# Kernel tuning notes

Hardware: AMD Instinct MI355X
Metric: run time of the kernel (lower is better)

Reference implementation:

```python
import jax, jax.numpy as jnp
import numpy as np

HIDDEN = 4096
N_HEADS = 16
HEAD_DIM = HIDDEN // N_HEADS  # 256
ROTARY_DIM = 64
MAX_POS = 2048
INIT_RANGE = 0.02


def _create_sinusoidal_positions(num_pos, dim):
    inv_freq = 1.0 / 10000 ** (np.arange(0, dim, 2) / dim)
    sinusoid_inp = np.einsum('i,j->ij', np.arange(num_pos), inv_freq).astype('float32')
    sin, cos = np.sin(sinusoid_inp), np.cos(sinusoid_inp)
    sentinel = dim // 2 + dim % 2
    out = np.zeros((num_pos, dim), dtype=np.float32)
    out[:, :sentinel] = sin
    out[:, sentinel:] = cos
    return jnp.array(out)

EMBED_POSITIONS = _create_sinusoidal_positions(MAX_POS, ROTARY_DIM)  # [MAX_POS, ROTARY_DIM]


def _rotate_every_two(t):
    # t: [B,S,H,R] -> interleaved (-x1, x0, -x3, x2, ...)
    rot = jnp.stack((-t[..., 1::2], t[..., ::2]), axis=-1)
    return rot.reshape(rot.shape[:-2] + (-1,))


def _apply_rotary(t, sin, cos):
    # sin/cos: [B,S,R/2] -> element-wise repeat x2 along last axis -> [B,S,1,R]
    sin_p = jnp.repeat(sin[:, :, None, :], 2, axis=-1)
    cos_p = jnp.repeat(cos[:, :, None, :], 2, axis=-1)
    return t * cos_p + _rotate_every_two(t) * sin_p


def setup_inputs() -> dict:
    key = jax.random.key(0)
    k0, k1, k2, k3, k4 = jax.random.split(key, 5)
    B, S = 2, 2048
    hidden_states = jax.random.normal(k0, (B, S, HIDDEN), dtype=jnp.float32)
    attention_mask = jnp.ones((B, S), dtype=jnp.float32)
    position_ids = jnp.broadcast_to(jnp.arange(S, dtype=jnp.int32), (B, S))
    Wq = jax.random.normal(k1, (HIDDEN, HIDDEN), dtype=jnp.float32) * INIT_RANGE
    Wk = jax.random.normal(k2, (HIDDEN, HIDDEN), dtype=jnp.float32) * INIT_RANGE
    Wv = jax.random.normal(k3, (HIDDEN, HIDDEN), dtype=jnp.float32) * INIT_RANGE
    Wo = jax.random.normal(k4, (HIDDEN, HIDDEN), dtype=jnp.float32) * INIT_RANGE
    return {"hidden_states": hidden_states, "attention_mask": attention_mask,
            "position_ids": position_ids, "Wq": Wq, "Wk": Wk, "Wv": Wv, "Wo": Wo}


def reference(hidden_states, attention_mask, position_ids, Wq, Wk, Wv, Wo):
    B, S, _ = hidden_states.shape
    # QKV projections (no bias), split heads -> [B,S,H,D]
    q = (hidden_states @ Wq).reshape(B, S, N_HEADS, HEAD_DIM)
    k = (hidden_states @ Wk).reshape(B, S, N_HEADS, HEAD_DIM)
    v = (hidden_states @ Wv).reshape(B, S, N_HEADS, HEAD_DIM)

    sincos = jnp.take(EMBED_POSITIONS, position_ids, axis=0)  # [B,S,ROTARY_DIM]
    sin, cos = jnp.split(sincos, 2, axis=-1)

    # Interleaved RoPE on first ROTARY_DIM channels only
    q_rot = _apply_rotary(q[..., :ROTARY_DIM], sin, cos)
    k_rot = _apply_rotary(k[..., :ROTARY_DIM], sin, cos)
    q = jnp.concatenate([q_rot, q[..., ROTARY_DIM:]], axis=-1)
    k = jnp.concatenate([k_rot, k[..., ROTARY_DIM:]], axis=-1)

    # Combined causal + padding mask -> additive bias
    causal = jnp.tril(jnp.ones((S, S), dtype=bool))[None, None]          # [1,1,S,S]
    pad = (attention_mask > 0)[:, None, None, :]                          # [B,1,1,S]
    mask = causal & pad                                                    # [B,1,S,S]
    bias = jnp.where(mask, 0.0, jnp.finfo(jnp.float32).min).astype(jnp.float32)

    # Scaled dot-product attention (query pre-scaled, as in flax dpa_weights)
    q = q / jnp.sqrt(jnp.float32(HEAD_DIM))
    scores = jnp.einsum('bqhd,bkhd->bhqk', q, k) + bias
    attn = jax.nn.softmax(scores, axis=-1)
    out = jnp.einsum('bhqk,bkhd->bqhd', attn, v).reshape(B, S, HIDDEN)
    return out @ Wo
```

## Files before the change

### kernel.cpp

```cpp
#include <hip/hip_runtime.h>


typedef unsigned short u16;
typedef __attribute__((ext_vector_type(4))) float f32x4;
typedef __attribute__((ext_vector_type(8))) short s16x8;
typedef __attribute__((ext_vector_type(4))) unsigned short u16x4;

#define HID 4096
#define SEQ 2048
#define NMAT (4096ull * 4096ull)

__device__ __forceinline__ u16 f2bf(float x) {
  unsigned int u = __builtin_bit_cast(unsigned int, x);
  u += 0x7FFFu + ((u >> 16) & 1u);
  return (u16)(u >> 16);
}
__device__ __forceinline__ float bf2f(u16 x) {
  unsigned int u = ((unsigned int)x) << 16;
  return __builtin_bit_cast(float, u);
}
__device__ __forceinline__ void cp16(const void* g, void* l) {
  __builtin_amdgcn_global_load_lds((__attribute__((address_space(1))) void*)(g),
                                   (__attribute__((address_space(3))) void*)(l),
                                   16, 0, 0);
}

__global__ __launch_bounds__(256) void k_cvt(const float* __restrict__ src,
                                             u16* __restrict__ dst) {
  size_t i = ((size_t)blockIdx.x * 256 + threadIdx.x) * 8;
  f32x4 a = *(const f32x4*)(src + i);
  f32x4 b = *(const f32x4*)(src + i + 4);
  u16x4 o0, o1;
  o0[0] = f2bf(a[0]); o0[1] = f2bf(a[1]); o0[2] = f2bf(a[2]); o0[3] = f2bf(a[3]);
  o1[0] = f2bf(b[0]); o1[1] = f2bf(b[1]); o1[2] = f2bf(b[2]); o1[3] = f2bf(b[3]);
  *(u16x4*)(dst + i) = o0;
  *(u16x4*)(dst + i + 4) = o1;
}

__global__ __launch_bounds__(256) void k_wtrans(const float* __restrict__ W0,
                                                const float* __restrict__ W1,
                                                const float* __restrict__ W2,
                                                const float* __restrict__ W3,
                                                u16* __restrict__ WT) {
  int z = blockIdx.z;
  const float* W = (z == 0) ? W0 : (z == 1) ? W1 : (z == 2) ? W2 : W3;
  u16* T = WT + (size_t)z * NMAT;
  __shared__ u16 tile[64][70];
  int t = threadIdx.x, tx = t & 15, ty = t >> 4;
  int n0 = blockIdx.x * 64, k0 = blockIdx.y * 64;
  for (int i = 0; i < 4; i++) {
    int kl = ty + 16 * i;
    f32x4 v = *(const f32x4*)(W + (size_t)(k0 + kl) * HID + n0 + tx * 4);
    tile[kl][tx * 4 + 0] = f2bf(v[0]);
    tile[kl][tx * 4 + 1] = f2bf(v[1]);
    tile[kl][tx * 4 + 2] = f2bf(v[2]);
    tile[kl][tx * 4 + 3] = f2bf(v[3]);
  }
  __syncthreads();
  for (int i = 0; i < 4; i++) {
    int nl = ty + 16 * i;
    u16x4 o;
    o[0] = tile[tx * 4 + 0][nl];
    o[1] = tile[tx * 4 + 1][nl];
    o[2] = tile[tx * 4 + 2][nl];
    o[3] = tile[tx * 4 + 3][nl];
    *(u16x4*)(T + (size_t)(n0 + nl) * HID + k0 + tx * 4) = o;
  }
}

__global__ __launch_bounds__(256) void k_vtrans(const u16* __restrict__ V,
                                                u16* __restrict__ Vt) {
  int bh = blockIdx.z, b = bh >> 4, h = bh & 15;
  int tok0 = blockIdx.x * 64, d0 = blockIdx.y * 64;
  __shared__ u16 tile[64][70];
  int t = threadIdx.x, tx = t & 15, ty = t >> 4;
  for (int i = 0; i < 4; i++) {
    int tl = ty + 16 * i;
    u16x4 v = *(const u16x4*)(V + (size_t)(b * SEQ + tok0 + tl) * HID + h * 256 + d0 + tx * 4);
    tile[tl][tx * 4 + 0] = v[0];
    tile[tl][tx * 4 + 1] = v[1];
    tile[tl][tx * 4 + 2] = v[2];
    tile[tl][tx * 4 + 3] = v[3];
  }
  __syncthreads();
  for (int i = 0; i < 4; i++) {
    int dl = ty + 16 * i;
    u16x4 o;
    o[0] = tile[tx * 4 + 0][dl];
    o[1] = tile[tx * 4 + 1][dl];
    o[2] = tile[tx * 4 + 2][dl];
    o[3] = tile[tx * 4 + 3][dl];
    *(u16x4*)(Vt + ((size_t)bh * 256 + d0 + dl) * SEQ + tok0 + tx * 4) = o;
  }
}

template <bool QKV>
__global__ __launch_bounds__(512, 2) void k_gemm8(const u16* __restrict__ A,
                                                  const u16* __restrict__ Bt0,
                                                  u16* __restrict__ Cb0,
                                                  float* __restrict__ Cf) {
  __shared__ u16 lds[65536];
  char* lds8 = (char*)lds;
  const int t = threadIdx.x, lane = t & 63, w = t >> 6;
  const int wm = w >> 2, wn = w & 3;
  const int l15 = lane & 15, g = lane >> 4;
  int lin = blockIdx.y * 16 + blockIdx.x;
  int swz = (lin & 7) * 32 + (lin >> 3);
  const int bm = (swz >> 4) * 256, bn = (swz & 15) * 256;
  const u16* Bt = Bt0;
  u16* Cb = Cb0;
  float scale = 1.f;
  if (QKV) {
    int z = blockIdx.z;
    Bt += (size_t)z * NMAT;
    Cb += (size_t)z * NMAT;
    if (z == 0) scale = 0.0625f;
  }
  const int Px = (t * 16) ^ (((t >> 5) & 1) << 5);
  const int r_s = Px >> 6, c_s = (Px & 63) >> 1;
  const u16* gA0 = A + (size_t)(bm + r_s) * HID + c_s;
  const u16* gA1 = gA0 + 128ull * HID;
  const u16* gB0 = Bt + (size_t)(bn + r_s) * HID + c_s;
  const u16* gB1 = gB0 + 128ull * HID;
  char* stA = lds8 + w * 1024;
  char* stB = lds8 + 32768 + w * 1024;
  const int sb = ((l15 >> 3) & 1) << 5;
  const int aL0 = wm * 16384 + ((l15 * 64 + g * 16) ^ sb);
  const int bL0 = 32768 + (wn >> 1) * 16384 + ((((wn & 1) * 64 + l15) * 64 + g * 16) ^ sb);
  const int aL1 = aL0 + 65536, bL1 = bL0 + 65536;

  f32x4 acc[8][4] = {};
  s16x8 af[4][2], b0[2][2], b1[2][2];

#define STG(P, D, KT) { const u16* s_ = (P) + (size_t)(KT) * 64; \
                        cp16(s_, (D)); cp16(s_ + 32, (D) + 8192); }
#define LDA8(MH, AL) \
  _Pragma("unroll") for (int mi = 0; mi < 4; mi++) { \
    af[mi][0] = *(const s16x8*)(lds8 + (AL) + (MH) * 4096 + mi * 1024); \
    af[mi][1] = *(const s16x8*)(lds8 + (AL) + (MH) * 4096 + mi * 1024 + 8192); }
#define LDB8(BQ, NH, BL) \
  _Pragma("unroll") for (int n2 = 0; n2 < 2; n2++) { \
    BQ[n2][0] = *(const s16x8*)(lds8 + (BL) + ((NH) * 2 + n2) * 1024); \
    BQ[n2][1] = *(const s16x8*)(lds8 + (BL) + ((NH) * 2 + n2) * 1024 + 8192); }
#define MM8(MH, BQ, NH) \
  _Pragma("unroll") for (int mi = 0; mi < 4; mi++) \
  _Pragma("unroll") for (int n2 = 0; n2 < 2; n2++) { \
    acc[(MH)*4+mi][(NH)*2+n2] = __builtin_amdgcn_mfma_f32_16x16x32_bf16( \
        af[mi][0], BQ[n2][0], acc[(MH)*4+mi][(NH)*2+n2], 0, 0, 0); \
    acc[(MH)*4+mi][(NH)*2+n2] = __builtin_amdgcn_mfma_f32_16x16x32_bf16( \
        af[mi][1], BQ[n2][1], acc[(MH)*4+mi][(NH)*2+n2], 0, 0, 0); }
#define BAR() __builtin_amdgcn_s_barrier()
#define LGKM0() asm volatile("s_waitcnt lgkmcnt(0)" ::: "memory")
#define PRIO1() __builtin_amdgcn_s_setprio(1)
#define PRIO0() __builtin_amdgcn_s_setprio(0)

  STG(gB0, stB, 0); STG(gB1, stB + 16384, 0);
  STG(gA0, stA, 0); STG(gA1, stA + 16384, 0);
  STG(gB0, stB + 65536, 1); STG(gB1, stB + 65536 + 16384, 1);
  asm volatile("s_waitcnt vmcnt(4)" ::: "memory");
  BAR();

  for (int it = 0; it < 32; ++it) {
    const int k1 = 2 * it + 1;
    const int k2 = (2 * it + 2 < 64) ? 2 * it + 2 : 63;
    const int k3 = (2 * it + 3 < 64) ? 2 * it + 3 : 63;
    LDA8(0, aL0); LDB8(b0, 0, bL0); STG(gA0, stA + 65536, k1);
    BAR(); LGKM0(); PRIO1(); MM8(0, b0, 0); PRIO0(); BAR();
    LDB8(b1, 1, bL0); STG(gA1, stA + 65536 + 16384, k1);
    BAR(); LGKM0(); PRIO1(); MM8(0, b1, 1); PRIO0(); BAR();
    LDA8(1, aL0); STG(gB0, stB, k2);
    BAR(); LGKM0(); PRIO1(); MM8(1, b1, 1); PRIO0(); BAR();
    STG(gB1, stB + 16384, k2);
    BAR(); PRIO1(); MM8(1, b0, 0); PRIO0();
    asm volatile("s_waitcnt vmcnt(4)" ::: "memory");
    BAR();
    LDA8(0, aL1); LDB8(b0, 0, bL1); STG(gA0, stA, k2);
    BAR(); LGKM0(); PRIO1(); MM8(0, b0, 0); PRIO0(); BAR();
    LDB8(b1, 1, bL1); STG(gA1, stA + 16384, k2);
    BAR(); LGKM0(); PRIO1(); MM8(0, b1, 1); PRIO0(); BAR();
    LDA8(1, aL1); STG(gB0, stB + 65536, k3);
    BAR(); LGKM0(); PRIO1(); MM8(1, b1, 1); PRIO0(); BAR();
    STG(gB1, stB + 65536 + 16384, k3);
    BAR(); PRIO1(); MM8(1, b0, 0); PRIO0();
    asm volatile("s_waitcnt vmcnt(4)" ::: "memory");
    BAR();
  }
  asm volatile("s_waitcnt vmcnt(0)" ::: "memory");
#pragma unroll
  for (int mi = 0; mi < 8; mi++)
#pragma unroll
    for (int ni = 0; ni < 4; ni++) {
      const int ml = bm + wm * 128 + mi * 16 + g * 4;
      const int nl = bn + wn * 64 + ni * 16 + l15;
#pragma unroll
      for (int rr = 0; rr < 4; rr++) {
        float v = acc[mi][ni][rr];
        if (QKV)
          Cb[(size_t)(ml + rr) * HID + nl] = f2bf(v * scale);
        else
          Cf[(size_t)(ml + rr) * HID + nl] = v;
      }
    }
#undef STG
#undef LDA8
#undef LDB8
#undef MM8
#undef BAR
#undef LGKM0
#undef PRIO1
#undef PRIO0
}

__global__ __launch_bounds__(256) void k_rope(u16* __restrict__ Q, u16* __restrict__ K,
                                              const int* __restrict__ pid) {
  int i = blockIdx.x * 256 + threadIdx.x;
  int m = i >> 9, rem = i & 511, h = rem >> 5, p = rem & 31;
  int pos = pid[m];
  double inv = pow(10000.0, -(double)p / 32.0);
  double ang = (double)pos * inv;
  float sv = (float)sin(ang), cv = (float)cos(ang);
  size_t idx = (size_t)m * HID + h * 256 + 2 * p;
  {
    unsigned int qp = *(const unsigned int*)(Q + idx);
    float a = bf2f((u16)qp), b = bf2f((u16)(qp >> 16));
    unsigned int o = (unsigned int)f2bf(a * cv - b * sv) |
                     ((unsigned int)f2bf(b * cv + a * sv) << 16);
    *(unsigned int*)(Q + idx) = o;
  }
  {
    unsigned int kp = *(const unsigned int*)(K + idx);
    float a = bf2f((u16)kp), b = bf2f((u16)(kp >> 16));
    unsigned int o = (unsigned int)f2bf(a * cv - b * sv) |
                     ((unsigned int)f2bf(b * cv + a * sv) << 16);
    *(unsigned int*)(K + idx) = o;
  }
}

__global__ __launch_bounds__(256, 2) void k_flash(const u16* __restrict__ Q,
                                                  const u16* __restrict__ Kg,
                                                  const u16* __restrict__ Vt,
                                                  const float* __restrict__ am,
                                                  u16* __restrict__ O) {
  __shared__ u16 smem[36864];
  u16* sK = smem;
  u16* sV = smem + 16384;
  u16* sP = smem + 32768;
  const int t = threadIdx.x, lane = t & 63, w = t >> 6;
  const int qt = gridDim.x - 1 - blockIdx.x;
  const int q0 = qt * 64;
  const int bh = blockIdx.y, b = bh >> 4, h = bh & 15;
  const size_t tokb = (size_t)b * SEQ;
  const int ch0 = h * 256;

  for (int j = 0; j < 8; j++) {
    int fc = j * 256 + t;
    int r = fc >> 5, cs = fc & 31, cg = cs ^ (r & 7);
    cp16(Q + (tokb + q0 + r) * (size_t)HID + ch0 + cg * 8, sK + j * 2048 + w * 512);
  }
  __syncthreads();
  s16x8 qf[8];
  {
    int rq = w * 16 + (lane & 15);
    for (int kf = 0; kf < 8; kf++) {
      int cs = ((lane >> 4) + 4 * kf) ^ (rq & 7);
      qf[kf] = *(const s16x8*)(sK + rq * 256 + cs * 8);
    }
  }
  f32x4 oacc[16] = {};
  float mrow[4], lrow[4];
  for (int rr = 0; rr < 4; rr++) { mrow[rr] = -1e30f; lrow[rr] = 0.f; }

  const int ntiles = qt + 1;
  for (int it = 0; it < ntiles; it++) {
    const int kt0 = it * 64;
    __syncthreads();
    for (int j = 0; j < 8; j++) {
      int fc = j * 256 + t;
      int r = fc >> 5, cs = fc & 31, cg = cs ^ (r & 7);
      cp16(Kg + (tokb + kt0 + r) * (size_t)HID + ch0 + cg * 8, sK + j * 2048 + w * 512);
    }
    for (int j = 0; j < 8; j++) {
      int fc = j * 256 + t;
      int rd = fc >> 3, cs = fc & 7, cg = cs ^ (rd & 7);
      cp16(Vt + ((size_t)bh * 256 + rd) * SEQ + kt0 + cg * 8, sV + j * 2048 + w * 512);
    }
    __syncthreads();
    f32x4 sacc[4] = {};
    for (int kf = 0; kf < 8; kf++) {
      s16x8 bf[4];
      for (int ni = 0; ni < 4; ni++) {
        int rk = ni * 16 + (lane & 15);
        int cs = ((lane >> 4) + 4 * kf) ^ (rk & 7);
        bf[ni] = *(const s16x8*)(sK + rk * 256 + cs * 8);
      }
      for (int ni = 0; ni < 4; ni++)
        sacc[ni] = __builtin_amdgcn_mfma_f32_16x16x32_bf16(qf[kf], bf[ni], sacc[ni], 0, 0, 0);
    }
    float amv[4];
    for (int ni = 0; ni < 4; ni++) amv[ni] = am[b * SEQ + kt0 + ni * 16 + (lane & 15)];
    const bool tail = (kt0 + 64 > q0);
    {
      int rbase = q0 + w * 16 + ((lane >> 4) << 2);
      for (int ni = 0; ni < 4; ni++) {
        int colg = kt0 + ni * 16 + (lane & 15);
        bool dead = (amv[ni] <= 0.f);
        for (int rr = 0; rr < 4; rr++)
          if (dead || (tail && colg > rbase + rr)) sacc[ni][rr] = -1e30f;
      }
    }
    float alpha[4];
    for (int rr = 0; rr < 4; rr++) {
      float v = fmaxf(fmaxf(sacc[0][rr], sacc[1][rr]),
                      fmaxf(sacc[2][rr], sacc[3][rr]));
      v = fmaxf(v, __shfl_xor(v, 1));
      v = fmaxf(v, __shfl_xor(v, 2));
      v = fmaxf(v, __shfl_xor(v, 4));
      v = fmaxf(v, __shfl_xor(v, 8));
      float mnew = fmaxf(mrow[rr], v);
      alpha[rr] = __expf(mrow[rr] - mnew);
      mrow[rr] = mnew;
    }
    for (int ni = 0; ni < 4; ni++)
      for (int rr = 0; rr < 4; rr++)
        sacc[ni][rr] = __expf(sacc[ni][rr] - mrow[rr]);
    for (int rr = 0; rr < 4; rr++) {
      float sm = sacc[0][rr] + sacc[1][rr] + sacc[2][rr] + sacc[3][rr];
      sm += __shfl_xor(sm, 1);
      sm += __shfl_xor(sm, 2);
      sm += __shfl_xor(sm, 4);
      sm += __shfl_xor(sm, 8);
      lrow[rr] = lrow[rr] * alpha[rr] + sm;
    }
    for (int nd = 0; nd < 16; nd++)
      for (int rr = 0; rr < 4; rr++) oacc[nd][rr] *= alpha[rr];
    for (int ni = 0; ni < 4; ni++) {
      int ktl = ni * 16 + (lane & 15);
      for (int rr = 0; rr < 4; rr++) {
        int pq = w * 16 + ((lane >> 4) << 2) + rr;
        int cs = (ktl >> 3) ^ (pq & 7);
        sP[pq * 64 + cs * 8 + (ktl & 7)] = f2bf(sacc[ni][rr]);
      }
    }
    for (int kf2 = 0; kf2 < 2; kf2++) {
      s16x8 pa;
      {
        int pq = w * 16 + (lane & 15);
        int cs = ((lane >> 4) + 4 * kf2) ^ (pq & 7);
        pa = *(const s16x8*)(sP + pq * 64 + cs * 8);
      }
      for (int nd = 0; nd < 16; nd++) {
        int rd = nd * 16 + (lane & 15);
        int cs = ((lane >> 4) + 4 * kf2) ^ (rd & 7);
        s16x8 vb = *(const s16x8*)(sV + rd * 64 + cs * 8);
        oacc[nd] = __builtin_amdgcn_mfma_f32_16x16x32_bf16(pa, vb, oacc[nd], 0, 0, 0);
      }
    }
  }
  {
    float rl[4];
    for (int rr = 0; rr < 4; rr++) rl[rr] = (lrow[rr] > 0.f) ? 1.f / lrow[rr] : 0.f;
    for (int nd = 0; nd < 16; nd++)
      for (int rr = 0; rr < 4; rr++) {
        size_t row = tokb + q0 + w * 16 + ((lane >> 4) << 2) + rr;
        O[row * HID + ch0 + nd * 16 + (lane & 15)] = f2bf(oacc[nd][rr] * rl[rr]);
      }
  }
}

extern "C" void kernel_launch(void* const* d_in, const int* in_sizes, int n_in,
                              void* d_out, int out_size, void* d_ws, size_t ws_size,
                              hipStream_t stream) {
  const float* hs = (const float*)d_in[0];
  const float* am = (const float*)d_in[1];
  const int* pid = (const int*)d_in[2];
  const float* Wq = (const float*)d_in[3];
  const float* Wk = (const float*)d_in[4];
  const float* Wv = (const float*)d_in[5];
  const float* Wo = (const float*)d_in[6];
  float* out = (float*)d_out;

  u16* wsp = (u16*)d_ws;
  u16* hsb = wsp;
  u16* WT = wsp + NMAT;
  u16* Qb = wsp + 5 * NMAT;
  u16* Kb = wsp + 6 * NMAT;
  u16* Vb = wsp + 7 * NMAT;
  u16* Vt = wsp + 1 * NMAT;
  u16* attn = hsb;

  k_cvt<<<8192, 256, 0, stream>>>(hs, hsb);
  k_wtrans<<<dim3(64, 64, 4), 256, 0, stream>>>(Wq, Wk, Wv, Wo, WT);
  k_gemm8<true><<<dim3(16, 16, 3), 512, 0, stream>>>(hsb, WT, Qb, nullptr);
  k_rope<<<8192, 256, 0, stream>>>(Qb, Kb, pid);
  k_vtrans<<<dim3(32, 4, 32), 256, 0, stream>>>(Vb, Vt);
  k_flash<<<dim3(32, 32), 256, 0, stream>>>(Qb, Kb, Vt, am, attn);
  k_gemm8<false><<<dim3(16, 16, 1), 512, 0, stream>>>(attn, WT + 3 * NMAT, nullptr, out);
}
```

Measured before the change: 1.032 ms.

## Software-pipeline LDS fragment loads ahead of MFMA in the GEMM main loop

The GEMM main loop now double-buffers the A fragments in registers (afA/afB). It issues LDS reads for the next sub-step before running the current MFMA block, and the explicit lgkmcnt(0) waits are replaced by sched_barrier fences. The aim is to hide LDS read latency behind matrix-core work instead of stalling before each MFMA group. The cost is extra VGPRs for the second A fragment buffer, which can raise register pressure or cause spills. The wait placement now relies on the compiler's inserted waitcnts.

```diff
diff --git a/kernel.cpp b/kernel.cpp
--- a/kernel.cpp
+++ b/kernel.cpp
@@ -130,60 +130,67 @@
   const int aL1 = aL0 + 65536, bL1 = bL0 + 65536;
 
   f32x4 acc[8][4] = {};
-  s16x8 af[4][2], b0[2][2], b1[2][2];
+  s16x8 afA[4][2], afB[4][2], b0[2][2], b1[2][2];
 
 #define STG(P, D, KT) { const u16* s_ = (P) + (size_t)(KT) * 64; \
                         cp16(s_, (D)); cp16(s_ + 32, (D) + 8192); }
-#define LDA8(MH, AL) \
+#define LDA8(DST, MH, AL) \
   _Pragma("unroll") for (int mi = 0; mi < 4; mi++) { \
-    af[mi][0] = *(const s16x8*)(lds8 + (AL) + (MH) * 4096 + mi * 1024); \
-    af[mi][1] = *(const s16x8*)(lds8 + (AL) + (MH) * 4096 + mi * 1024 + 8192); }
-#define LDB8(BQ, NH, BL) \
+    DST[mi][0] = *(const s16x8*)(lds8 + (AL) + (MH) * 4096 + mi * 1024); \
+    DST[mi][1] = *(const s16x8*)(lds8 + (AL) + (MH) * 4096 + mi * 1024 + 8192); }
+#define LDB8(DST, NH, BL) \
   _Pragma("unroll") for (int n2 = 0; n2 < 2; n2++) { \
-    BQ[n2][0] = *(const s16x8*)(lds8 + (BL) + ((NH) * 2 + n2) * 1024); \
-    BQ[n2][1] = *(const s16x8*)(lds8 + (BL) + ((NH) * 2 + n2) * 1024 + 8192); }
-#define MM8(MH, BQ, NH) \
+    DST[n2][0] = *(const s16x8*)(lds8 + (BL) + ((NH) * 2 + n2) * 1024); \
+    DST[n2][1] = *(const s16x8*)(lds8 + (BL) + ((NH) * 2 + n2) * 1024 + 8192); }
+#define MM8(AF, BQ, MH, NH) \
   _Pragma("unroll") for (int mi = 0; mi < 4; mi++) \
   _Pragma("unroll") for (int n2 = 0; n2 < 2; n2++) { \
     acc[(MH)*4+mi][(NH)*2+n2] = __builtin_amdgcn_mfma_f32_16x16x32_bf16( \
-        af[mi][0], BQ[n2][0], acc[(MH)*4+mi][(NH)*2+n2], 0, 0, 0); \
+        AF[mi][0], BQ[n2][0], acc[(MH)*4+mi][(NH)*2+n2], 0, 0, 0); \
     acc[(MH)*4+mi][(NH)*2+n2] = __builtin_amdgcn_mfma_f32_16x16x32_bf16( \
-        af[mi][1], BQ[n2][1], acc[(MH)*4+mi][(NH)*2+n2], 0, 0, 0); }
+        AF[mi][1], BQ[n2][1], acc[(MH)*4+mi][(NH)*2+n2], 0, 0, 0); }
 #define BAR() __builtin_amdgcn_s_barrier()
-#define LGKM0() asm volatile("s_waitcnt lgkmcnt(0)" ::: "memory")
+#define SBAR0() __builtin_amdgcn_sched_barrier(0)
 #define PRIO1() __builtin_amdgcn_s_setprio(1)
 #define PRIO0() __builtin_amdgcn_s_setprio(0)
+#define VMC4() asm volatile("s_waitcnt vmcnt(4)" ::: "memory")
 
   STG(gB0, stB, 0); STG(gB1, stB + 16384, 0);
   STG(gA0, stA, 0); STG(gA1, stA + 16384, 0);
   STG(gB0, stB + 65536, 1); STG(gB1, stB + 65536 + 16384, 1);
-  asm volatile("s_waitcnt vmcnt(4)" ::: "memory");
+  VMC4();
   BAR();
+  LDA8(afA, 0, aL0); LDB8(b0, 0, bL0);
+  SBAR0();
 
   for (int it = 0; it < 32; ++it) {
     const int k1 = 2 * it + 1;
     const int k2 = (2 * it + 2 < 64) ? 2 * it + 2 : 63;
     const int k3 = (2 * it + 3 < 64) ? 2 * it + 3 : 63;
-    LDA8(0, aL0); LDB8(b0, 0, bL0); STG(gA0, stA + 65536, k1);
-    BAR(); LGKM0(); PRIO1(); MM8(0, b0, 0); PRIO0(); BAR();
-    LDB8(b1, 1, bL0); STG(gA1, stA + 65536 + 16384, k1);
-    BAR(); LGKM0(); PRIO1(); MM8(0, b1, 1); PRIO0(); BAR();
-    LDA8(1, aL0); STG(gB0, stB, k2);
-    BAR(); LGKM0(); PRIO1(); MM8(1, b1, 1); PRIO0(); BAR();
+    STG(gA0, stA + 65536, k1);
+    LDB8(b1, 1, bL0); SBAR0(); LDA8(afB, 1, aL0); SBAR0();
+    BAR(); PRIO1(); MM8(afA, b0, 0, 0); PRIO0(); BAR();
+    STG(gA1, stA + 65536 + 16384, k1);
+    BAR(); PRIO1(); MM8(afA, b1, 0, 1); PRIO0(); BAR();
+    STG(gB0, stB, k2);
+    BAR(); PRIO1(); MM8(afB, b0, 1, 0); PRIO0(); BAR();
     STG(gB1, stB + 16384, k2);
-    BAR(); PRIO1(); MM8(1, b0, 0); PRIO0();
-    asm volatile("s_waitcnt vmcnt(4)" ::: "memory");
+    VMC4();
     BAR();
-    LDA8(0, aL1); LDB8(b0, 0, bL1); STG(gA0, stA, k2);
-    BAR(); LGKM0(); PRIO1(); MM8(0, b0, 0); PRIO0(); BAR();
-    LDB8(b1, 1, bL1); STG(gA1, stA + 16384, k2);
-    BAR(); LGKM0(); PRIO1(); MM8(0, b1, 1); PRIO0(); BAR();
-    LDA8(1, aL1); STG(gB0, stB + 65536, k3);
-    BAR(); LGKM0(); PRIO1(); MM8(1, b1, 1); PRIO0(); BAR();
+    LDA8(afA, 0, aL1); LDB8(b0, 0, bL1); SBAR0();
+    PRIO1(); MM8(afB, b1, 1, 1); PRIO0(); BAR();
+    STG(gA0, stA, k2);
+    LDB8(b1, 1, bL1); SBAR0(); LDA8(afB, 1, aL1); SBAR0();
+    BAR(); PRIO1(); MM8(afA, b0, 0, 0); PRIO0(); BAR();
+    STG(gA1, stA + 16384, k2);
+    BAR(); PRIO1(); MM8(afA, b1, 0, 1); PRIO0(); BAR();
+    STG(gB0, stB + 65536, k3);
+    BAR(); PRIO1(); MM8(afB, b0, 1, 0); PRIO0(); BAR();
     STG(gB1, stB + 65536 + 16384, k3);
-    BAR(); PRIO1(); MM8(1, b0, 0); PRIO0();
-    asm volatile("s_waitcnt vmcnt(4)" ::: "memory");
+    VMC4();
     BAR();
+    LDA8(afA, 0, aL0); LDB8(b0, 0, bL0); SBAR0();
+    PRIO1(); MM8(afB, b1, 1, 1); PRIO0(); BAR();
   }
   asm volatile("s_waitcnt vmcnt(0)" ::: "memory");
 #pragma unroll
@@ -206,9 +213,10 @@
 #undef LDB8
 #undef MM8
 #undef BAR
-#undef LGKM0
+#undef SBAR0
 #undef PRIO1
 #undef PRIO0
+#undef VMC4
 }
 
 __global__ __launch_bounds__(256) void k_rope(u16* __restrict__ Q, u16* __restrict__ K,
```

Result: slower. 1.110 ms (+7.6%).
